# Kernel optimization log

Measured on AMD Instinct MI355X. Metric: run time of the kernel, lower is better.

The kernel has to match this reference:

```python
import jax, jax.numpy as jnp
import numpy as np

ETA = 0.01   # Hebbian learning rate of the plasticity rule
LR = 1.0     # CircuitModel.lr


def setup_inputs() -> dict:
    key = jax.random.key(0)
    k1, k2, k3 = jax.random.split(key, 3)
    B, T, NI, NO, NOBS = 64, 256, 512, 512, 128
    X = jax.random.normal(k1, (B, T, NI), dtype=jnp.float32)
    W_init = jax.random.normal(k2, (B, NO, NI), dtype=jnp.float32) * 0.1
    observed_idx = jnp.sort(jax.random.randint(k3, (NOBS,), 0, NO))
    return {"X": X, "W_init": W_init, "observed_idx": observed_idx}


def reference(X, W_init, observed_idx):
    # X: [B,T,NI], W_init: [B,NO,NI], observed_idx: [NOBS] int
    NO = W_init.shape[1]
    mask = jnp.zeros((NO,), X.dtype).at[observed_idx].set(1.0)  # [NO]

    def step(W, x_t):
        # x_t: [B,NI]
        pre = jnp.einsum('boi,bi->bo', W, x_t)          # [B,NO]
        y = jax.nn.sigmoid(pre)
        m = y[:, observed_idx]                           # [B,NOBS] recorded before masking
        y_sparse = y * mask                              # zero unobserved outputs
        W = W * mask[None, :, None]                      # zero unobserved rows of W
        dW = ETA * (y_sparse[:, :, None] * x_t[:, None, :])  # Hebbian outer product
        return W + LR * dW, m

    _, m_traj = jax.lax.scan(step, W_init, jnp.swapaxes(X, 0, 1))  # [T,B,NOBS]
    return jnp.swapaxes(m_traj, 0, 1)  # [B,T,NOBS]
```

## Files before the change

### kernel.cpp

```cpp
#include <hip/hip_runtime.h>

#define NB   64
#define NT   256
#define NI   512
#define NO   512
#define NOBS 128
#define ETA  0.01f

typedef __attribute__((ext_vector_type(8))) short bf16x8;
typedef __attribute__((ext_vector_type(4))) float f32x4;

#define X4_COUNT  (NB*NT*NI/4)
#define WG4_COUNT (NB*NOBS*NI/4)
#define K0_TOTAL  (X4_COUNT + WG4_COUNT)

__device__ __forceinline__ unsigned short f2bf(float f) {
    unsigned int u = __float_as_uint(f);
    return (unsigned short)((u + 0x7fffu + ((u >> 16) & 1u)) >> 16);
}

__global__ __launch_bounds__(256)
void k0_convert(const float* __restrict__ X, const float* __restrict__ Wi,
                const int* __restrict__ obs,
                unsigned short* __restrict__ Xb, unsigned short* __restrict__ Wg)
{
    int idx = blockIdx.x * 256 + threadIdx.x;
    const int stride = gridDim.x * 256;
    for (; idx < K0_TOTAL; idx += stride) {
        float4 v; ushort4* dst;
        if (idx < X4_COUNT) {
            v = ((const float4*)X)[idx];
            dst = (ushort4*)Xb + idx;
        } else {
            int g = idx - X4_COUNT;
            int row = g >> 7, pos = g & 127;
            int b = row >> 7, j = row & 127;
            v = ((const float4*)(Wi + ((size_t)b * NO + obs[j]) * NI))[pos];
            dst = (ushort4*)Wg + ((size_t)row * 128 + pos);
        }
        *dst = make_ushort4(f2bf(v.x), f2bf(v.y), f2bf(v.z), f2bf(v.w));
    }
}

__global__ __launch_bounds__(256)
void k1_gemm(const unsigned short* __restrict__ Xb,
             const unsigned short* __restrict__ Wg,
             float* __restrict__ Gd, unsigned short* __restrict__ Gh,
             float* __restrict__ P0)
{
    __shared__ unsigned short As[128 * 64];
    __shared__ unsigned short Bs[128 * 64];

    const int tid  = threadIdx.x;
    const int lane = tid & 63;
    const int wv   = tid >> 6;
    const int l16  = lane & 15;
    const int quad = lane >> 4;

    const int b   = blockIdx.x & 63;
    const int sub = blockIdx.x >> 6;

    const unsigned short* xbB = Xb + (size_t)b * NT * NI;
    const unsigned short *aRows, *bRows;
    int bm = 0, bn = 0;
    if (sub < 3) {
        bm = (sub >= 1) ? 1 : 0;
        bn = (sub == 2) ? 1 : 0;
        aRows = xbB + (size_t)bm * 128 * NI;
        bRows = xbB + (size_t)bn * 128 * NI;
    } else {
        const int pb = sub - 3;
        bm = pb;
        aRows = xbB + (size_t)pb * 128 * NI;
        bRows = Wg + (size_t)b * NOBS * NI;
    }

    const int wm = (wv >> 1) * 64;
    const int wn = (wv & 1) * 64;

    f32x4 acc[4][4] = {};

    for (int kb = 0; kb < NI / 64; ++kb) {
        __syncthreads();
#pragma unroll
        for (int it = 0; it < 4; ++it) {
            const int s = it * 256 + tid;
            const int m = s >> 3, c = s & 7;
            const int slot = m * 64 + ((c ^ (m & 7)) * 8);
            const size_t goff = (size_t)m * NI + kb * 64 + c * 8;
            *(bf16x8*)&As[slot] = *(const bf16x8*)(aRows + goff);
            *(bf16x8*)&Bs[slot] = *(const bf16x8*)(bRows + goff);
        }
        __syncthreads();
#pragma unroll
        for (int ks = 0; ks < 2; ++ks) {
            const int q = ks * 4 + quad;
            bf16x8 af[4], bfr[4];
#pragma unroll
            for (int mt = 0; mt < 4; ++mt) {
                const int m = wm + mt * 16 + l16;
                af[mt] = *(const bf16x8*)&As[m * 64 + ((q ^ (m & 7)) * 8)];
            }
#pragma unroll
            for (int nt = 0; nt < 4; ++nt) {
                const int n = wn + nt * 16 + l16;
                bfr[nt] = *(const bf16x8*)&Bs[n * 64 + ((q ^ (n & 7)) * 8)];
            }
#pragma unroll
            for (int mt = 0; mt < 4; ++mt)
#pragma unroll
                for (int nt = 0; nt < 4; ++nt)
                    acc[mt][nt] = __builtin_amdgcn_mfma_f32_16x16x32_bf16(
                        af[mt], bfr[nt], acc[mt][nt], 0, 0, 0);
        }
    }

    if (sub < 3) {
        unsigned short* GhB = Gh + ((size_t)b << 16);
        float* GdB = Gd + ((size_t)b << 12);
#pragma unroll
        for (int mt = 0; mt < 4; ++mt)
#pragma unroll
            for (int nt = 0; nt < 4; ++nt) {
                const int gcol = bn * 128 + wn + nt * 16 + l16;
#pragma unroll
                for (int r = 0; r < 4; ++r) {
                    const int grow = bm * 128 + wm + mt * 16 + quad * 4 + r;
                    const float v = acc[mt][nt][r];
                    GhB[(size_t)grow * 256 + gcol] = f2bf(v);
                    if ((grow >> 4) == (gcol >> 4))
                        GdB[((grow >> 4) << 8) + ((grow & 15) << 4) + (gcol & 15)] = v;
                }
            }
    } else {
        float* Pb = P0 + (size_t)b * NT * NOBS + (size_t)bm * 128 * NOBS;
#pragma unroll
        for (int mt = 0; mt < 4; ++mt)
#pragma unroll
            for (int nt = 0; nt < 4; ++nt)
#pragma unroll
                for (int r = 0; r < 4; ++r)
                    Pb[(size_t)(wm + mt * 16 + quad * 4 + r) * NOBS
                       + wn + nt * 16 + l16] = acc[mt][nt][r];
    }
}

__global__ __launch_bounds__(512)
void k2_scan(const float* __restrict__ Gd, const unsigned short* __restrict__ Gh,
             const float* __restrict__ P0, float* __restrict__ out)
{
    __shared__ float gdiag[16 * 16 * 16];
    __shared__ float preS[16 * 32];
    __shared__ unsigned int ybf2[2 * 8 * 32];

    const int tid  = threadIdx.x;
    const int lane = tid & 63;
    const int l16  = lane & 15;
    const int quad = lane >> 4;
    const int w    = __builtin_amdgcn_readfirstlane(tid >> 6);

    const int b  = blockIdx.x & 63;
    const int jg = blockIdx.x >> 6;

    const float* Pb = P0 + (size_t)b * NT * NOBS + jg * 32;
    const unsigned short* GhB = Gh + ((size_t)b << 16);
    float* ob = out + (size_t)b * NT * NOBS + jg * 32;

    {
        const f32x4* gs = (const f32x4*)(Gd + ((size_t)b << 12));
        ((f32x4*)gdiag)[tid]       = gs[tid];
        ((f32x4*)gdiag)[512 + tid] = gs[512 + tid];
    }

    f32x4 acc[2][2];
#pragma unroll
    for (int s2 = 0; s2 < 2; ++s2)
#pragma unroll
        for (int nt = 0; nt < 2; ++nt)
#pragma unroll
            for (int r = 0; r < 4; ++r)
                acc[s2][nt][r] =
                    Pb[(size_t)(w * 32 + s2 * 16 + quad * 4 + r) * NOBS
                       + nt * 16 + l16];

#pragma unroll
    for (int c = 0; c < 16; ++c) {
        const int cp = c & 1;
        if (w == (c >> 1)) {
#pragma unroll
            for (int nt = 0; nt < 2; ++nt)
#pragma unroll
                for (int r = 0; r < 4; ++r)
                    preS[(quad * 4 + r) * 32 + nt * 16 + l16] = acc[cp][nt][r];
        }
        __syncthreads();
        if (w == (c >> 1) && lane < 32) {
            const int j = lane;
            float p[16];
#pragma unroll
            for (int u = 0; u < 16; ++u) p[u] = preS[u * 32 + j];
            const float* gdc = gdiag + c * 256;
            float eprev = 0.f;
#pragma unroll
            for (int u = 0; u < 16; ++u) {
                const float y = 1.f / (1.f + __expf(-p[u]));
                ob[(size_t)(c * 16 + u) * NOBS + j] = y;
                const float e = ETA * y;
#pragma unroll
                for (int v = u + 1; v < 16; ++v)
                    p[v] = fmaf(e, gdc[u * 16 + v], p[v]);
                if (u & 1)
                    ybf2[cp * 256 + (u >> 1) * 32 + j] =
                        (unsigned)f2bf(eprev) | ((unsigned)f2bf(e) << 16);
                else
                    eprev = e;
            }
        }
        __syncthreads();
        if (c < 15) {
            union { bf16x8 v; unsigned int d[4]; } B0, B1;
#pragma unroll
            for (int p2 = 0; p2 < 4; ++p2) { B0.d[p2] = 0; B1.d[p2] = 0; }
            if (quad < 2) {
#pragma unroll
                for (int p2 = 0; p2 < 4; ++p2) {
                    B0.d[p2] = ybf2[cp * 256 + (quad * 4 + p2) * 32 + l16];
                    B1.d[p2] = ybf2[cp * 256 + (quad * 4 + p2) * 32 + 16 + l16];
                }
            }
#pragma unroll
            for (int s2 = 0; s2 < 2; ++s2) {
                const int T = 2 * w + s2;
                if (T > c) {
                    union { bf16x8 v; unsigned int d[4]; } A;
#pragma unroll
                    for (int p2 = 0; p2 < 4; ++p2) A.d[p2] = 0;
                    if (quad < 2)
                        A.v = *(const bf16x8*)(GhB + (size_t)(T * 16 + l16) * 256
                                               + c * 16 + quad * 8);
                    acc[s2][0] = __builtin_amdgcn_mfma_f32_16x16x32_bf16(
                        A.v, B0.v, acc[s2][0], 0, 0, 0);
                    acc[s2][1] = __builtin_amdgcn_mfma_f32_16x16x32_bf16(
                        A.v, B1.v, acc[s2][1], 0, 0, 0);
                }
            }
        }
    }
}

extern "C" void kernel_launch(void* const* d_in, const int* in_sizes, int n_in,
                              void* d_out, int out_size, void* d_ws, size_t ws_size,
                              hipStream_t stream)
{
    const float* X   = (const float*)d_in[0];
    const float* Wi  = (const float*)d_in[1];
    const int*   obs = (const int*)d_in[2];
    float*       out = (float*)d_out;

    float*          Gd = (float*)d_ws;
    float*          P0 = (float*)((char*)d_ws + (1u << 20));
    unsigned short* Gh = (unsigned short*)((char*)d_ws + (9u << 20));
    unsigned short* Xb = (unsigned short*)((char*)d_ws + (17u << 20));
    unsigned short* Wg = (unsigned short*)((char*)d_ws + (33u << 20));

    hipLaunchKernelGGL(k0_convert, dim3(3072), dim3(256), 0, stream,
                       X, Wi, obs, Xb, Wg);
    hipLaunchKernelGGL(k1_gemm, dim3(NB * 5), dim3(256), 0, stream,
                       Xb, Wg, Gd, Gh, P0);
    hipLaunchKernelGGL(k2_scan, dim3(NB * 4), dim3(512), 0, stream,
                       Gd, Gh, P0, out);
}
```

Measured before the change: 166.7 us.

## Split scan columns finer, fuse chunk scan into MFMA loop with prefetch

The scan kernel now gives each block 16 observed columns instead of 32, doubling the grid to 512 blocks, and requests higher occupancy through launch bounds. The next chunk's scan is run by the owning wave right after its MFMA update, inside the same loop iteration, which removes one barrier per chunk. The A fragments for the next chunk are prefetched from global memory while the current one is consumed. It also pads the preS array to avoid LDS bank conflicts and uses a fast reciprocal in the sigmoid. The trade-off is that each block reloads the diagonal tiles and fragments for half as many columns, so redundant global traffic doubles. The wait-count-only handoff within a wave also relies on that wave's LDS ordering.

```diff
diff --git a/kernel.cpp b/kernel.cpp
--- a/kernel.cpp
+++ b/kernel.cpp
@@ -145,13 +145,13 @@
     }
 }
 
-__global__ __launch_bounds__(512)
+__global__ __launch_bounds__(512, 4)
 void k2_scan(const float* __restrict__ Gd, const unsigned short* __restrict__ Gh,
              const float* __restrict__ P0, float* __restrict__ out)
 {
     __shared__ float gdiag[16 * 16 * 16];
-    __shared__ float preS[16 * 32];
-    __shared__ unsigned int ybf2[2 * 8 * 32];
+    __shared__ float preS[16 * 17];
+    __shared__ unsigned int ybf2[2 * 8 * 16];
 
     const int tid  = threadIdx.x;
     const int lane = tid & 63;
@@ -162,9 +162,9 @@
     const int b  = blockIdx.x & 63;
     const int jg = blockIdx.x >> 6;
 
-    const float* Pb = P0 + (size_t)b * NT * NOBS + jg * 32;
+    const float* Pb = P0 + (size_t)b * NT * NOBS + jg * 16;
     const unsigned short* GhB = Gh + ((size_t)b << 16);
-    float* ob = out + (size_t)b * NT * NOBS + jg * 32;
+    float* ob = out + (size_t)b * NT * NOBS + jg * 16;
 
     {
         const f32x4* gs = (const f32x4*)(Gd + ((size_t)b << 12));
@@ -172,79 +172,93 @@
         ((f32x4*)gdiag)[512 + tid] = gs[512 + tid];
     }
 
-    f32x4 acc[2][2];
+    f32x4 acc[2];
 #pragma unroll
     for (int s2 = 0; s2 < 2; ++s2)
 #pragma unroll
-        for (int nt = 0; nt < 2; ++nt)
-#pragma unroll
-            for (int r = 0; r < 4; ++r)
-                acc[s2][nt][r] =
-                    Pb[(size_t)(w * 32 + s2 * 16 + quad * 4 + r) * NOBS
-                       + nt * 16 + l16];
-
-#pragma unroll
-    for (int c = 0; c < 16; ++c) {
-        const int cp = c & 1;
-        if (w == (c >> 1)) {
-#pragma unroll
-            for (int nt = 0; nt < 2; ++nt)
-#pragma unroll
-                for (int r = 0; r < 4; ++r)
-                    preS[(quad * 4 + r) * 32 + nt * 16 + l16] = acc[cp][nt][r];
-        }
-        __syncthreads();
-        if (w == (c >> 1) && lane < 32) {
+        for (int r = 0; r < 4; ++r)
+            acc[s2][r] = Pb[(size_t)(w * 32 + s2 * 16 + quad * 4 + r) * NOBS + l16];
+
+    const int T0 = 2 * w, T1 = 2 * w + 1;
+
+    union AB { bf16x8 v; unsigned int d[4]; };
+    AB Acur0, Acur1, Anext0, Anext1;
+#pragma unroll
+    for (int p2 = 0; p2 < 4; ++p2) {
+        Acur0.d[p2] = 0; Acur1.d[p2] = 0; Anext0.d[p2] = 0; Anext1.d[p2] = 0;
+    }
+    if (quad < 2) {
+        if (T0 > 0)
+            Acur0.v = *(const bf16x8*)(GhB + (size_t)(T0 * 16 + l16) * 256 + quad * 8);
+        Acur1.v = *(const bf16x8*)(GhB + (size_t)(T1 * 16 + l16) * 256 + quad * 8);
+    }
+
+    auto scan_chunk = [&](const int c, const f32x4 a) {
+#pragma unroll
+        for (int r = 0; r < 4; ++r)
+            preS[(quad * 4 + r) * 17 + l16] = a[r];
+        asm volatile("s_waitcnt lgkmcnt(0)" ::: "memory");
+        if (lane < 16) {
             const int j = lane;
+            const int cp = c & 1;
             float p[16];
 #pragma unroll
-            for (int u = 0; u < 16; ++u) p[u] = preS[u * 32 + j];
+            for (int u = 0; u < 16; ++u) p[u] = preS[u * 17 + j];
             const float* gdc = gdiag + c * 256;
             float eprev = 0.f;
 #pragma unroll
             for (int u = 0; u < 16; ++u) {
-                const float y = 1.f / (1.f + __expf(-p[u]));
+                const float y = __builtin_amdgcn_rcpf(1.f + __expf(-p[u]));
                 ob[(size_t)(c * 16 + u) * NOBS + j] = y;
                 const float e = ETA * y;
 #pragma unroll
                 for (int v = u + 1; v < 16; ++v)
                     p[v] = fmaf(e, gdc[u * 16 + v], p[v]);
                 if (u & 1)
-                    ybf2[cp * 256 + (u >> 1) * 32 + j] =
+                    ybf2[cp * 128 + (u >> 1) * 16 + j] =
                         (unsigned)f2bf(eprev) | ((unsigned)f2bf(e) << 16);
                 else
                     eprev = e;
             }
         }
+    };
+
+    if (w == 0)
+        scan_chunk(0, acc[0]);
+    __syncthreads();
+
+#pragma unroll
+    for (int c = 0; c < 15; ++c) {
+        if (T1 > c) {
+            AB B;
+#pragma unroll
+            for (int p2 = 0; p2 < 4; ++p2) B.d[p2] = 0;
+            if (quad < 2) {
+#pragma unroll
+                for (int p2 = 0; p2 < 4; ++p2)
+                    B.d[p2] = ybf2[(c & 1) * 128 + (quad * 4 + p2) * 16 + l16];
+            }
+#pragma unroll
+            for (int p2 = 0; p2 < 4; ++p2) { Anext0.d[p2] = 0; Anext1.d[p2] = 0; }
+            if (quad < 2) {
+                if (T0 > c + 1)
+                    Anext0.v = *(const bf16x8*)(GhB + (size_t)(T0 * 16 + l16) * 256
+                                                + (c + 1) * 16 + quad * 8);
+                if (T1 > c + 1)
+                    Anext1.v = *(const bf16x8*)(GhB + (size_t)(T1 * 16 + l16) * 256
+                                                + (c + 1) * 16 + quad * 8);
+            }
+            if (T0 > c)
+                acc[0] = __builtin_amdgcn_mfma_f32_16x16x32_bf16(
+                    Acur0.v, B.v, acc[0], 0, 0, 0);
+            acc[1] = __builtin_amdgcn_mfma_f32_16x16x32_bf16(
+                Acur1.v, B.v, acc[1], 0, 0, 0);
+            if (w == ((c + 1) >> 1))
+                scan_chunk(c + 1, acc[(c + 1) & 1]);
+            Acur0 = Anext0;
+            Acur1 = Anext1;
+        }
         __syncthreads();
-        if (c < 15) {
-            union { bf16x8 v; unsigned int d[4]; } B0, B1;
-#pragma unroll
-            for (int p2 = 0; p2 < 4; ++p2) { B0.d[p2] = 0; B1.d[p2] = 0; }
-            if (quad < 2) {
-#pragma unroll
-                for (int p2 = 0; p2 < 4; ++p2) {
-                    B0.d[p2] = ybf2[cp * 256 + (quad * 4 + p2) * 32 + l16];
-                    B1.d[p2] = ybf2[cp * 256 + (quad * 4 + p2) * 32 + 16 + l16];
-                }
-            }
-#pragma unroll
-            for (int s2 = 0; s2 < 2; ++s2) {
-                const int T = 2 * w + s2;
-                if (T > c) {
-                    union { bf16x8 v; unsigned int d[4]; } A;
-#pragma unroll
-                    for (int p2 = 0; p2 < 4; ++p2) A.d[p2] = 0;
-                    if (quad < 2)
-                        A.v = *(const bf16x8*)(GhB + (size_t)(T * 16 + l16) * 256
-                                               + c * 16 + quad * 8);
-                    acc[s2][0] = __builtin_amdgcn_mfma_f32_16x16x32_bf16(
-                        A.v, B0.v, acc[s2][0], 0, 0, 0);
-                    acc[s2][1] = __builtin_amdgcn_mfma_f32_16x16x32_bf16(
-                        A.v, B1.v, acc[s2][1], 0, 0, 0);
-                }
-            }
-        }
     }
 }
 
@@ -267,6 +281,6 @@
                        X, Wi, obs, Xb, Wg);
     hipLaunchKernelGGL(k1_gemm, dim3(NB * 5), dim3(256), 0, stream,
                        Xb, Wg, Gd, Gh, P0);
-    hipLaunchKernelGGL(k2_scan, dim3(NB * 4), dim3(512), 0, stream,
+    hipLaunchKernelGGL(k2_scan, dim3(NB * 8), dim3(512), 0, stream,
                        Gd, Gh, P0, out);
 }
```

Result: faster. 158.2 us (-5.1%).
